# Kernel optimization log

Hardware: AMD Instinct MI355X
Metric: run time of the kernel (lower is better)

Reference implementation:

```python
import jax, jax.numpy as jnp
import numpy as np

CFG = {"dt": 1.0, "T_r": 2.0, "kappa_j": 1.0, "tau_j": 10.0, "gamma_m": 1.0, "R_m": 1.0,
       "tau_m": 20.0, "thresh": 1.0, "tau_tr": 20.0, "tau_data": 10.0,
       "alpha_gen": 0.5, "alpha_disc": 0.5}


def _lif(v, x, tr, j, refrac, ti, cfg):
    """One LIF update for a hidden layer (bPC_SNNLayer.update_state)."""
    dt = cfg["dt"]
    j = j + dt / cfg["tau_j"] * (-cfg["kappa_j"] * j + ti)
    is_refr = refrac > 0
    v_next = v + dt / cfg["tau_m"] * (-cfg["gamma_m"] * v + cfg["R_m"] * j)
    v = jnp.where(is_refr, v, v_next)
    spikes = (v > cfg["thresh"]).astype(v.dtype) * (1.0 - is_refr.astype(v.dtype))
    v = v * (1.0 - spikes)
    refrac = jnp.maximum(refrac - dt, 0.0)
    refrac = jnp.where(spikes > 0, jnp.asarray(cfg["T_r"], v.dtype), refrac)
    tr = tr - tr / cfg["tau_tr"] + spikes  # spike trace (layer.x)
    return v, spikes, tr, j, refrac


def _forward(x_data, y_target, W0, W1, W2, V0, V1, V2, num_steps):
    cfg = CFG
    B = x_data.shape[0]
    d0, d1, d2, d3 = x_data.shape[1], W0.shape[1], W1.shape[1], W2.shape[1]
    dt_ = x_data.dtype
    z = lambda d: jnp.zeros((B, d), dt_)
    state = dict(v1=z(d1), tr1=z(d1), j1=z(d1), r1=z(d1), s1=z(d1),
                 v2=z(d2), tr2=z(d2), j2=z(d2), r2=z(d2), s2=z(d2),
                 eg0=z(d0), eg1=z(d1), eg2=z(d2),
                 ed1=z(d1), ed2=z(d2), ed3=z(d3),
                 z_data=z(d0), z_label=z(d3))
    ag, ad = cfg["alpha_gen"], cfg["alpha_disc"]

    def step(st, _):
        # phase 1: currents into hidden layers 1 and 2 (layers 0/3 are data/label, no-op)
        ti1 = -st["eg1"] + st["ed2"] @ V1 - st["ed1"] + st["eg0"] @ W0
        ti2 = -st["eg2"] + st["ed3"] @ V2 - st["ed2"] + st["eg1"] @ W1
        v1, s1, tr1, j1, r1 = _lif(st["v1"], st["tr1"], st["tr1"], st["j1"], st["r1"], ti1, cfg) if False else _lif(st["v1"], st["tr1"], st["tr1"], st["j1"], st["r1"], ti1, cfg)
        v1, s1, tr1, j1, r1 = _lif(st["v1"], st["tr1"], st["tr1"], st["j1"], st["r1"], ti1, cfg)
        v2, s2, tr2, j2, r2 = _lif(st["v2"], st["tr2"], st["tr2"], st["j2"], st["r2"], ti2, cfg)
        # phase 2: error recomputation (training mode with label clamped)
        z_data = st["z_data"] - st["z_data"] / cfg["tau_data"] + x_data
        z_label = st["z_label"] - st["z_label"] / cfg["tau_data"] + y_target
        eg0 = ag * (z_data - s1 @ W0.T)          # layer 0 generative error
        ed1 = ad * (tr1 - x_data @ V0.T)          # layer 1 discriminative error
        eg1 = ag * (tr1 - s2 @ W1.T)
        ed2 = ad * (tr2 - s1 @ V1.T)
        eg2 = ag * (tr2 - y_target @ W2.T)        # top hidden: label-clamped generative target
        ed3 = ad * (z_label - s2 @ V2.T)          # label layer discriminative error
        return dict(v1=v1, tr1=tr1, j1=j1, r1=r1, s1=s1,
                    v2=v2, tr2=tr2, j2=j2, r2=r2, s2=s2,
                    eg0=eg0, eg1=eg1, eg2=eg2, ed1=ed1, ed2=ed2, ed3=ed3,
                    z_data=z_data, z_label=z_label), None

    final, _ = jax.lax.scan(step, state, None, length=num_steps)
    return final["ed3"]


def setup_inputs() -> dict:
    key = jax.random.key(0)
    ks = jax.random.split(key, 8)
    B = 128
    sizes = (2048, 4096, 4096, 512)
    sc = 0.02  # weight scale kept small so dynamics stay numerically sane over 16 steps
    return {
        "x_data": jax.random.normal(ks[0], (B, sizes[0]), jnp.float32),
        "y_target": jax.random.normal(ks[1], (B, sizes[3]), jnp.float32),
        "W0": jax.random.normal(ks[2], (sizes[0], sizes[1]), jnp.float32) * sc,
        "W1": jax.random.normal(ks[3], (sizes[1], sizes[2]), jnp.float32) * sc,
        "W2": jax.random.normal(ks[4], (sizes[2], sizes[3]), jnp.float32) * sc,
        "V0": jax.random.normal(ks[5], (sizes[1], sizes[0]), jnp.float32) * sc,
        "V1": jax.random.normal(ks[6], (sizes[2], sizes[1]), jnp.float32) * sc,
        "V2": jax.random.normal(ks[7], (sizes[3], sizes[2]), jnp.float32) * sc,
        "num_steps": 16,
    }


def reference(x_data, y_target, W0, W1, W2, V0, V1, V2, num_steps):
    return _forward(x_data, y_target, W0, W1, W2, V0, V1, V2, num_steps)
```

## Files before the change

kernel.cpp:

```cpp
#include <hip/hip_runtime.h>


#define DEVINL __device__ __forceinline__

using bf16x8 = __attribute__((ext_vector_type(8))) __bf16;
using f32x4  = __attribute__((ext_vector_type(4))) float;
using i32x4  = __attribute__((ext_vector_type(4))) int;
typedef unsigned char uchar;

static constexpr int BB = 128;
static constexpr int D0 = 2048, D1 = 4096, D2 = 4096, D3 = 512;
static constexpr int NSTEPS = 16;

struct Ctx {
  const float *x, *y, *W0, *W1, *W2, *V0, *V1, *V2;
  float *v1, *j1, *r1, *tr1, *v2, *j2, *r2, *tr2;
  float *zd, *zl, *xV0T, *yW2T;
  __bf16 *x_bf, *y_bf, *eg0_bf, *eg1_bf, *ed2_bf, *ed3_bf;
  uchar *s1_f8, *s2_f8, *WA8, *WB8;
  __bf16 *W0t, *W1t, *V1t, *V2t, *V0n, *W2n;
  float *out;
};

DEVINL void gload16(const void* g, void* l) {
  __builtin_amdgcn_global_load_lds(
      (const __attribute__((address_space(1))) void*)g,
      (__attribute__((address_space(3))) void*)l, 16, 0, 0);
}
DEVINL uint32_t lds_off(const void* p) {
  return (uint32_t)(uintptr_t)(__attribute__((address_space(3))) const void*)p;
}
DEVINL bf16x8 dsr128(uint32_t addr) {
  i32x4 r;
  asm volatile("ds_read_b128 %0, %1" : "=v"(r) : "v"(addr));
  return __builtin_bit_cast(bf16x8, r);
}
DEVINL long dsr64(uint32_t addr) {
  long r;
  asm volatile("ds_read_b64 %0, %1" : "=v"(r) : "v"(addr));
  return r;
}

struct Seg { const __bf16* A; unsigned ldA; const __bf16* W; unsigned ldW; int iters; };
struct SPtr { const __bf16 *a0, *a1, *w; };
struct SPtrW { const __bf16 *a, *w; };

DEVINL SPtr mkptr(const Seg& s, int t) {
  int r = t >> 3;
  int u = ((t & 7) ^ (r & 7)) * 8;
  SPtr p;
  p.a0 = s.A + (size_t)r * s.ldA + u;
  p.a1 = s.A + (size_t)(r + 32) * s.ldA + u;
  p.w  = s.W + (size_t)r * s.ldW + u;
  return p;
}
DEVINL SPtrW mkptrw(const Seg& s, int t) {
  int r = t >> 3;
  int u = ((t & 7) ^ (r & 7)) * 8;
  SPtrW p;
  p.a = s.A + (size_t)r * s.ldA + u;
  p.w = s.W + (size_t)r * s.ldW + u;
  return p;
}

DEVINL void run_gemm(const Seg* segs, int nIter, __bf16* lsA, __bf16* lsW,
                     int t, int wm, int wn, int l16, int lg, f32x4* acc) {
  const int seg0it = segs[0].iters;
  SPtr p = mkptr(segs[0], t);
  int nxt = 0;
  auto stage = [&](int s) {
    __bf16* bA = lsA + (s & 3) * 4096;
    __bf16* bW = lsW + (s & 3) * 2048;
    gload16(p.a0, bA + t * 8);
    gload16(p.a1, bA + 2048 + t * 8);
    gload16(p.w,  bW + t * 8);
    p.a0 += 64; p.a1 += 64; p.w += 64;
    if (++nxt == seg0it) p = mkptr(segs[1], t);
  };

  const int x7 = l16 & 7;
  uint32_t aB = lds_off(lsA), wB = lds_off(lsW);
  uint32_t aAd[2][2], wAd[2];
#pragma unroll
  for (int mt = 0; mt < 2; ++mt)
#pragma unroll
    for (int ks = 0; ks < 2; ++ks)
      aAd[mt][ks] = aB + (uint32_t)(wm * 32 + mt * 16 + l16) * 128u
                       + (uint32_t)(((ks * 4 + lg) ^ x7) * 16);
#pragma unroll
  for (int ks = 0; ks < 2; ++ks)
    wAd[ks] = wB + (uint32_t)(wn * 16 + l16) * 128u
                 + (uint32_t)(((ks * 4 + lg) ^ x7) * 16);

  auto compute = [&](int i) {
    uint32_t oa = (uint32_t)(i & 3) * 8192u, ow = (uint32_t)(i & 3) * 4096u;
    bf16x8 a00 = dsr128(aAd[0][0] + oa);
    bf16x8 a01 = dsr128(aAd[0][1] + oa);
    bf16x8 a10 = dsr128(aAd[1][0] + oa);
    bf16x8 a11 = dsr128(aAd[1][1] + oa);
    bf16x8 b0  = dsr128(wAd[0] + ow);
    bf16x8 b1  = dsr128(wAd[1] + ow);
    asm volatile("s_waitcnt lgkmcnt(0)" ::: "memory");
    __builtin_amdgcn_sched_barrier(0);
    __builtin_amdgcn_s_setprio(1);
    acc[0] = __builtin_amdgcn_mfma_f32_16x16x32_bf16(a00, b0, acc[0], 0, 0, 0);
    acc[1] = __builtin_amdgcn_mfma_f32_16x16x32_bf16(a10, b0, acc[1], 0, 0, 0);
    acc[0] = __builtin_amdgcn_mfma_f32_16x16x32_bf16(a01, b1, acc[0], 0, 0, 0);
    acc[1] = __builtin_amdgcn_mfma_f32_16x16x32_bf16(a11, b1, acc[1], 0, 0, 0);
    __builtin_amdgcn_s_setprio(0);
  };

  stage(0); stage(1); stage(2);
  for (int i = 0; i < nIter - 3; ++i) {
    asm volatile("s_waitcnt vmcnt(6)" ::: "memory");
    __builtin_amdgcn_s_barrier();
    stage(i + 3);
    compute(i);
  }
  asm volatile("s_waitcnt vmcnt(6)" ::: "memory");
  __builtin_amdgcn_s_barrier();
  compute(nIter - 3);
  asm volatile("s_waitcnt vmcnt(3)" ::: "memory");
  __builtin_amdgcn_s_barrier();
  compute(nIter - 2);
  asm volatile("s_waitcnt vmcnt(0)" ::: "memory");
  __builtin_amdgcn_s_barrier();
  compute(nIter - 1);
}

DEVINL void run_gemm128w(const Seg* segs, int nIter, __bf16* lsA, __bf16* lsW,
                         int t, int wm, int wn, int l16, int lg, f32x4* acc) {
  const int seg0it = segs[0].iters;
  SPtrW p = mkptrw(segs[0], t);
  int nxt = 0;
  auto stage = [&](int buf) {
    __bf16* bA = lsA + buf * 8192;
    __bf16* bW = lsW + buf * 8192;
    gload16(p.a,      bA + t * 8);
    gload16(p.a + 64, bA + 4096 + t * 8);
    gload16(p.w,      bW + t * 8);
    gload16(p.w + 64, bW + 4096 + t * 8);
    p.a += 128; p.w += 128;
    if (++nxt == seg0it) p = mkptrw(segs[1], t);
  };

  const int x7 = l16 & 7;
  uint32_t aB = lds_off(lsA), wB = lds_off(lsW);
  uint32_t aAd[2][2], wAd[2];
#pragma unroll
  for (int mt = 0; mt < 2; ++mt)
#pragma unroll
    for (int ks = 0; ks < 2; ++ks)
      aAd[mt][ks] = aB + (uint32_t)(wm * 32 + mt * 16 + l16) * 128u
                       + (uint32_t)(((ks * 4 + lg) ^ x7) * 16);
#pragma unroll
  for (int ks = 0; ks < 2; ++ks)
    wAd[ks] = wB + (uint32_t)(wn * 16 + l16) * 128u
                 + (uint32_t)(((ks * 4 + lg) ^ x7) * 16);

  auto compute = [&](int buf) {
    uint32_t oa = (uint32_t)buf * 16384u, ow = (uint32_t)buf * 16384u;
    bf16x8 a00 = dsr128(aAd[0][0] + oa);
    bf16x8 a01 = dsr128(aAd[0][1] + oa);
    bf16x8 a10 = dsr128(aAd[1][0] + oa);
    bf16x8 a11 = dsr128(aAd[1][1] + oa);
    bf16x8 b0  = dsr128(wAd[0] + ow);
    bf16x8 b1  = dsr128(wAd[1] + ow);
    bf16x8 c00 = dsr128(aAd[0][0] + oa + 8192);
    bf16x8 c01 = dsr128(aAd[0][1] + oa + 8192);
    bf16x8 c10 = dsr128(aAd[1][0] + oa + 8192);
    bf16x8 c11 = dsr128(aAd[1][1] + oa + 8192);
    bf16x8 d0  = dsr128(wAd[0] + ow + 8192);
    bf16x8 d1  = dsr128(wAd[1] + ow + 8192);
    asm volatile("s_waitcnt lgkmcnt(0)" ::: "memory");
    __builtin_amdgcn_sched_barrier(0);
    __builtin_amdgcn_s_setprio(1);
    acc[0] = __builtin_amdgcn_mfma_f32_16x16x32_bf16(a00, b0, acc[0], 0, 0, 0);
    acc[1] = __builtin_amdgcn_mfma_f32_16x16x32_bf16(a10, b0, acc[1], 0, 0, 0);
    acc[0] = __builtin_amdgcn_mfma_f32_16x16x32_bf16(a01, b1, acc[0], 0, 0, 0);
    acc[1] = __builtin_amdgcn_mfma_f32_16x16x32_bf16(a11, b1, acc[1], 0, 0, 0);
    acc[0] = __builtin_amdgcn_mfma_f32_16x16x32_bf16(c00, d0, acc[0], 0, 0, 0);
    acc[1] = __builtin_amdgcn_mfma_f32_16x16x32_bf16(c10, d0, acc[1], 0, 0, 0);
    acc[0] = __builtin_amdgcn_mfma_f32_16x16x32_bf16(c01, d1, acc[0], 0, 0, 0);
    acc[1] = __builtin_amdgcn_mfma_f32_16x16x32_bf16(c11, d1, acc[1], 0, 0, 0);
    __builtin_amdgcn_s_setprio(0);
  };

  stage(0); stage(1);
  int cur = 0, nx = 2;
  for (int i = 0; i < nIter - 2; ++i) {
    asm volatile("s_waitcnt vmcnt(4)" ::: "memory");
    __builtin_amdgcn_s_barrier();
    stage(nx);
    compute(cur);
    cur = (cur == 2) ? 0 : cur + 1;
    nx  = (nx == 2) ? 0 : nx + 1;
  }
  asm volatile("s_waitcnt vmcnt(4)" ::: "memory");
  __builtin_amdgcn_s_barrier();
  compute(cur);
  cur = (cur == 2) ? 0 : cur + 1;
  asm volatile("s_waitcnt vmcnt(0)" ::: "memory");
  __builtin_amdgcn_s_barrier();
  compute(cur);
}


__global__ __launch_bounds__(512, 1) void phase1_v17(Ctx c, float edsc) {
  __shared__ __align__(16) __bf16 lsA[3][8192];
  __shared__ __align__(16) __bf16 lsW[3][8192];
  int t = threadIdx.x, w = t >> 6, l = t & 63;
  int l16 = l & 15, lg = l >> 4, wm = w >> 2, wn = w & 3;
  int bx = blockIdx.x;
  int z = bx >> 7, idx = bx & 127;
  int mh = idx >> 6, n0 = (idx & 63) * 64;
  f32x4 acc[2];
  f32x4 z4 = {0.f, 0.f, 0.f, 0.f};
  acc[0] = z4; acc[1] = z4;

  Seg segs[2]; int nIter, N;
  float *v, *j, *rf, *tr; const float* aux; const __bf16* buf; uchar* sf8;
  if (z == 0) {
    segs[0] = { c.ed2_bf + (size_t)mh * 64 * D2, (unsigned)D2, c.V1t + (size_t)n0 * D2, (unsigned)D2, 32 };
    segs[1] = { c.eg0_bf + (size_t)mh * 64 * D0, (unsigned)D0, c.W0t + (size_t)n0 * D0, (unsigned)D0, 16 };
    nIter = 48; N = D1;
    v = c.v1; j = c.j1; rf = c.r1; tr = c.tr1; buf = c.eg1_bf; aux = c.xV0T; sf8 = c.s1_f8;
  } else {
    segs[0] = { c.ed3_bf + (size_t)mh * 64 * D3, (unsigned)D3, c.V2t + (size_t)n0 * D3, (unsigned)D3, 4 };
    segs[1] = { c.eg1_bf + (size_t)mh * 64 * D1, (unsigned)D1, c.W1t + (size_t)n0 * D1, (unsigned)D1, 32 };
    nIter = 36; N = D2;
    v = c.v2; j = c.j2; rf = c.r2; tr = c.tr2; buf = c.ed2_bf; aux = c.yW2T; sf8 = c.s2_f8;
  }

  run_gemm128w(segs, nIter, &lsA[0][0], &lsW[0][0], t, wm, wn, l16, lg, acc);

  int n = n0 + wn * 16 + l16;
#pragma unroll
  for (int mt = 0; mt < 2; ++mt) {
#pragma unroll
    for (int r = 0; r < 4; ++r) {
      int b = mh * 64 + wm * 32 + mt * 16 + lg * 4 + r;
      size_t idx2 = (size_t)b * N + n;
      float to = tr[idx2];
      float ti = acc[mt][r] - (float)buf[idx2] - edsc * (to - aux[idx2]);
      float jo = j[idx2];
      float jn = jo + 0.1f * (ti - jo);
      float ro = rf[idx2];
      float vo = v[idx2];
      bool refr = ro > 0.0f;
      float vn = refr ? vo : (vo + 0.05f * (jn - vo));
      float sp = (!refr && vn > 1.0f) ? 1.0f : 0.0f;
      if (sp != 0.0f) vn = 0.0f;
      float rn = fmaxf(ro - 1.0f, 0.0f);
      if (sp != 0.0f) rn = 2.0f;
      float tn = to - 0.05f * to + sp;
      v[idx2] = vn; j[idx2] = jn; rf[idx2] = rn; tr[idx2] = tn;
      sf8[idx2] = (sp != 0.0f) ? (uchar)0x38 : (uchar)0;
    }
  }
}


__global__ __launch_bounds__(256, 2) void phase2_v15(Ctx c) {
  __shared__ __align__(128) uchar lsA[4][8192];
  __shared__ __align__(128) uchar lsW[4][8192];
  int t = threadIdx.x, w = t >> 6, l = t & 63;
  int l16 = l & 15, lg = l >> 4, wm = w >> 1, wn = w & 1;
  int g = blockIdx.x, mh = blockIdx.y;

  const uchar *A, *W; int n0; bool isA;
  if (g < 96) { isA = true;  A = c.s1_f8 + (size_t)mh * 64 * D1; W = c.WA8 + (size_t)g * 64 * 4096;        n0 = g * 64; }
  else        { isA = false; A = c.s2_f8 + (size_t)mh * 64 * D2; W = c.WB8 + (size_t)(g - 96) * 64 * 4096; n0 = (g - 96) * 64; }

  f32x4 acc[4];
  f32x4 z4 = {0.f, 0.f, 0.f, 0.f};
#pragma unroll
  for (int i = 0; i < 4; i++) acc[i] = z4;

  int row8 = t >> 3, u8 = t & 7;
  int su8 = (u8 ^ ((row8 >> 1) & 7)) * 16;
  const uchar* pA0 = A + (size_t)row8 * 4096 + su8;
  const uchar* pA1 = A + (size_t)(row8 + 32) * 4096 + su8;
  const uchar* pW0 = W + (size_t)row8 * 4096 + su8;
  const uchar* pW1 = W + (size_t)(row8 + 32) * 4096 + su8;
  uchar* dA = &lsA[0][0] + t * 16;
  uchar* dW = &lsW[0][0] + t * 16;
  auto stage = [&](int s) {
    uint32_t o = (uint32_t)(s & 3) * 8192u;
    gload16(pA0, dA + o);
    gload16(pA1, dA + o + 4096);
    gload16(pW0, dW + o);
    gload16(pW1, dW + o + 4096);
    pA0 += 128; pA1 += 128; pW0 += 128; pW1 += 128;
  };

  uint32_t aB = lds_off(lsA), wB = lds_off(lsW);
  uint32_t adA[2], adW[2];
#pragma unroll
  for (int mt = 0; mt < 2; ++mt) {
    int ra = wm * 32 + mt * 16 + l16;
    adA[mt] = aB + (uint32_t)ra * 128u
            + (uint32_t)((((lg >> 1) ^ ((ra >> 1) & 7)) * 16) + (lg & 1) * 8);
  }
#pragma unroll
  for (int nt = 0; nt < 2; ++nt) {
    int rw = wn * 32 + nt * 16 + l16;
    adW[nt] = wB + (uint32_t)rw * 128u
            + (uint32_t)((((lg >> 1) ^ ((rw >> 1) & 7)) * 16) + (lg & 1) * 8);
  }

  auto compute = [&](int i) {
    uint32_t off = (uint32_t)(i & 3) * 8192u;
    uint32_t A0 = adA[0] + off, A1 = adA[1] + off;
    uint32_t B0 = adW[0] + off, B1 = adW[1] + off;
    long a0v0 = dsr64(A0);         long a1v0 = dsr64(A1);
    long b0v0 = dsr64(B0);         long b1v0 = dsr64(B1);
    long a0v1 = dsr64(A0 ^ 32u);   long a1v1 = dsr64(A1 ^ 32u);
    long b0v1 = dsr64(B0 ^ 32u);   long b1v1 = dsr64(B1 ^ 32u);
    long a0v2 = dsr64(A0 ^ 64u);   long a1v2 = dsr64(A1 ^ 64u);
    long b0v2 = dsr64(B0 ^ 64u);   long b1v2 = dsr64(B1 ^ 64u);
    long a0v3 = dsr64(A0 ^ 96u);   long a1v3 = dsr64(A1 ^ 96u);
    long b0v3 = dsr64(B0 ^ 96u);   long b1v3 = dsr64(B1 ^ 96u);
    asm volatile("s_waitcnt lgkmcnt(0)" ::: "memory");
    __builtin_amdgcn_sched_barrier(0);
    __builtin_amdgcn_s_setprio(1);
    acc[0] = __builtin_amdgcn_mfma_f32_16x16x32_fp8_fp8(a0v0, b0v0, acc[0], 0, 0, 0);
    acc[1] = __builtin_amdgcn_mfma_f32_16x16x32_fp8_fp8(a0v0, b1v0, acc[1], 0, 0, 0);
    acc[2] = __builtin_amdgcn_mfma_f32_16x16x32_fp8_fp8(a1v0, b0v0, acc[2], 0, 0, 0);
    acc[3] = __builtin_amdgcn_mfma_f32_16x16x32_fp8_fp8(a1v0, b1v0, acc[3], 0, 0, 0);
    acc[0] = __builtin_amdgcn_mfma_f32_16x16x32_fp8_fp8(a0v1, b0v1, acc[0], 0, 0, 0);
    acc[1] = __builtin_amdgcn_mfma_f32_16x16x32_fp8_fp8(a0v1, b1v1, acc[1], 0, 0, 0);
    acc[2] = __builtin_amdgcn_mfma_f32_16x16x32_fp8_fp8(a1v1, b0v1, acc[2], 0, 0, 0);
    acc[3] = __builtin_amdgcn_mfma_f32_16x16x32_fp8_fp8(a1v1, b1v1, acc[3], 0, 0, 0);
    acc[0] = __builtin_amdgcn_mfma_f32_16x16x32_fp8_fp8(a0v2, b0v2, acc[0], 0, 0, 0);
    acc[1] = __builtin_amdgcn_mfma_f32_16x16x32_fp8_fp8(a0v2, b1v2, acc[1], 0, 0, 0);
    acc[2] = __builtin_amdgcn_mfma_f32_16x16x32_fp8_fp8(a1v2, b0v2, acc[2], 0, 0, 0);
    acc[3] = __builtin_amdgcn_mfma_f32_16x16x32_fp8_fp8(a1v2, b1v2, acc[3], 0, 0, 0);
    acc[0] = __builtin_amdgcn_mfma_f32_16x16x32_fp8_fp8(a0v3, b0v3, acc[0], 0, 0, 0);
    acc[1] = __builtin_amdgcn_mfma_f32_16x16x32_fp8_fp8(a0v3, b1v3, acc[1], 0, 0, 0);
    acc[2] = __builtin_amdgcn_mfma_f32_16x16x32_fp8_fp8(a1v3, b0v3, acc[2], 0, 0, 0);
    acc[3] = __builtin_amdgcn_mfma_f32_16x16x32_fp8_fp8(a1v3, b1v3, acc[3], 0, 0, 0);
    __builtin_amdgcn_s_setprio(0);
  };

  const int nIter = 32;
  stage(0); stage(1); stage(2);
  for (int i = 0; i < nIter - 3; ++i) {
    asm volatile("s_waitcnt vmcnt(8)" ::: "memory");
    __builtin_amdgcn_s_barrier();
    stage(i + 3);
    compute(i);
  }
  asm volatile("s_waitcnt vmcnt(8)" ::: "memory");
  __builtin_amdgcn_s_barrier();
  compute(nIter - 3);
  asm volatile("s_waitcnt vmcnt(4)" ::: "memory");
  __builtin_amdgcn_s_barrier();
  compute(nIter - 2);
  asm volatile("s_waitcnt vmcnt(0)" ::: "memory");
  __builtin_amdgcn_s_barrier();
  compute(nIter - 1);

#pragma unroll
  for (int mt = 0; mt < 2; ++mt)
#pragma unroll
    for (int nt = 0; nt < 2; ++nt) {
      int nn = n0 + wn * 32 + nt * 16 + l16;
#pragma unroll
      for (int r = 0; r < 4; ++r) {
        int b = mh * 64 + wm * 32 + mt * 16 + lg * 4 + r;
        float av = acc[mt * 2 + nt][r];
        if (isA) {
          if (nn < 2048) {
            size_t idx = (size_t)b * D0 + nn;
            float zo = c.zd[idx]; float zn = zo - 0.1f * zo + c.x[idx];
            c.zd[idx] = zn;
            c.eg0_bf[idx] = (__bf16)(0.5f * (zn - av));
          } else {
            size_t idx = (size_t)b * D2 + (nn - 2048);
            c.ed2_bf[idx] = (__bf16)(0.5f * (c.tr2[idx] - av));
          }
        } else {
          if (nn < 4096) {
            size_t idx = (size_t)b * D1 + nn;
            c.eg1_bf[idx] = (__bf16)(0.5f * (c.tr1[idx] - av));
          } else {
            size_t idx = (size_t)b * D3 + (nn - 4096);
            float zo = c.zl[idx]; float zn = zo - 0.1f * zo + c.y[idx];
            c.zl[idx] = zn;
            float e = 0.5f * (zn - av);
            c.out[idx] = e; c.ed3_bf[idx] = (__bf16)e;
          }
        }
      }
    }
}


__global__ __launch_bounds__(256, 2) void precomp_v6(Ctx c) {
  __shared__ __align__(16) __bf16 lsA[4][4096];
  __shared__ __align__(16) __bf16 lsW[4][2048];
  int t = threadIdx.x, w = t >> 6, l = t & 63;
  int l16 = l & 15, lg = l >> 4, wm = w >> 1, wn = w & 1;
  int n0 = blockIdx.x * 32, mh = blockIdx.y;
  f32x4 acc[2];
  f32x4 z4 = {0.f, 0.f, 0.f, 0.f};
  acc[0] = z4; acc[1] = z4;

  Seg segs[2]; int nIter, N; float* outp;
  if (blockIdx.z == 0) {
    segs[0] = { c.x_bf + (size_t)mh * 64 * D0, (unsigned)D0, c.V0n + (size_t)n0 * D0, (unsigned)D0, 32 };
    nIter = 32; N = D1; outp = c.xV0T;
  } else {
    segs[0] = { c.y_bf + (size_t)mh * 64 * D3, (unsigned)D3, c.W2n + (size_t)n0 * D3, (unsigned)D3, 8 };
    nIter = 8; N = D2; outp = c.yW2T;
  }
  segs[1] = segs[0];

  run_gemm(segs, nIter, &lsA[0][0], &lsW[0][0], t, wm, wn, l16, lg, acc);

  int n = n0 + wn * 16 + l16;
#pragma unroll
  for (int mt = 0; mt < 2; ++mt)
#pragma unroll
    for (int r = 0; r < 4; ++r) {
      int b = mh * 64 + wm * 32 + mt * 16 + lg * 4 + r;
      outp[(size_t)b * N + n] = acc[mt][r];
    }
}


__global__ __launch_bounds__(256) void wprep_kernel(Ctx c, int g0) {
  __shared__ float ls[64][65];
  int g = blockIdx.x + g0;
  const float* src; __bf16* tp = nullptr; uchar* n8 = nullptr; __bf16* nb = nullptr; int R, C;
  if (g < 2048)       { src = c.W0; n8 = c.WA8;                         tp = c.W0t; R = D0; C = D1; }
  else if (g < 6144)  { g -= 2048;  src = c.W1; n8 = c.WB8;             tp = c.W1t; R = D1; C = D2; }
  else if (g < 10240) { g -= 6144;  src = c.V1; n8 = c.WA8 + (size_t)2048 * 4096; tp = c.V1t; R = D2; C = D1; }
  else if (g < 10752) { g -= 10240; src = c.V2; n8 = c.WB8 + (size_t)4096 * 4096; tp = c.V2t; R = D3; C = D2; }
  else if (g < 12800) { g -= 10752; src = c.V0; nb = c.V0n; R = D1; C = D0; }
  else                { g -= 12800; src = c.W2; nb = c.W2n; R = D2; C = D3; }
  int tpr = C / 64;
  int r0 = (g / tpr) * 64, c0 = (g % tpr) * 64;
  int t = threadIdx.x, r = t >> 2, q = t & 3;

  const float4* s4 = reinterpret_cast<const float4*>(src + (size_t)(r0 + r) * C + c0 + q * 16);
  if (n8) {
    int pk[4];
#pragma unroll
    for (int i = 0; i < 4; i++) {
      float4 v = s4[i];
      ls[r][q * 16 + i * 4 + 0] = v.x; ls[r][q * 16 + i * 4 + 1] = v.y;
      ls[r][q * 16 + i * 4 + 2] = v.z; ls[r][q * 16 + i * 4 + 3] = v.w;
      int wd = __builtin_amdgcn_cvt_pk_fp8_f32(v.x, v.y, 0, false);
      wd = __builtin_amdgcn_cvt_pk_fp8_f32(v.z, v.w, wd, true);
      pk[i] = wd;
    }
    int4 pv; pv.x = pk[0]; pv.y = pk[1]; pv.z = pk[2]; pv.w = pk[3];
    *reinterpret_cast<int4*>(n8 + (size_t)(r0 + r) * C + c0 + q * 16) = pv;
    __syncthreads();
    union { __bf16 h[16]; int4 qq[2]; } wv;
#pragma unroll
    for (int i = 0; i < 16; i++) wv.h[i] = (__bf16)ls[q * 16 + i][r];
    int4* dt = reinterpret_cast<int4*>(tp + (size_t)(c0 + r) * R + r0 + q * 16);
    dt[0] = wv.qq[0]; dt[1] = wv.qq[1];
  } else {
    union { __bf16 h[16]; int4 qq[2]; } uu;
#pragma unroll
    for (int i = 0; i < 4; i++) {
      float4 v = s4[i];
      uu.h[i * 4 + 0] = (__bf16)v.x; uu.h[i * 4 + 1] = (__bf16)v.y;
      uu.h[i * 4 + 2] = (__bf16)v.z; uu.h[i * 4 + 3] = (__bf16)v.w;
    }
    int4* dn = reinterpret_cast<int4*>(nb + (size_t)(r0 + r) * C + c0 + q * 16);
    dn[0] = uu.qq[0]; dn[1] = uu.qq[1];
  }
}

__global__ __launch_bounds__(256) void castinit_kernel(Ctx c) {
  int i = blockIdx.x * 256 + threadIdx.x;
  const int NX = BB * D0 / 4;
  union { __bf16 h[4]; uint2 u; } p, q;
  if (i < NX) {
    float4 xv = reinterpret_cast<const float4*>(c.x)[i];
    reinterpret_cast<float4*>(c.zd)[i] = xv;
    p.h[0] = (__bf16)xv.x; p.h[1] = (__bf16)xv.y; p.h[2] = (__bf16)xv.z; p.h[3] = (__bf16)xv.w;
    reinterpret_cast<uint2*>(c.x_bf)[i] = p.u;
    q.h[0] = (__bf16)(0.5f * xv.x); q.h[1] = (__bf16)(0.5f * xv.y);
    q.h[2] = (__bf16)(0.5f * xv.z); q.h[3] = (__bf16)(0.5f * xv.w);
    reinterpret_cast<uint2*>(c.eg0_bf)[i] = q.u;
  } else {
    int k = i - NX;
    float4 yv = reinterpret_cast<const float4*>(c.y)[k];
    reinterpret_cast<float4*>(c.zl)[k] = yv;
    p.h[0] = (__bf16)yv.x; p.h[1] = (__bf16)yv.y; p.h[2] = (__bf16)yv.z; p.h[3] = (__bf16)yv.w;
    reinterpret_cast<uint2*>(c.y_bf)[k] = p.u;
    q.h[0] = (__bf16)(0.5f * yv.x); q.h[1] = (__bf16)(0.5f * yv.y);
    q.h[2] = (__bf16)(0.5f * yv.z); q.h[3] = (__bf16)(0.5f * yv.w);
    reinterpret_cast<uint2*>(c.ed3_bf)[k] = q.u;
  }
}


extern "C" void kernel_launch(void* const* d_in, const int* in_sizes, int n_in,
                              void* d_out, int out_size, void* d_ws, size_t ws_size,
                              hipStream_t stream) {
  Ctx c;
  c.x  = (const float*)d_in[0];
  c.y  = (const float*)d_in[1];
  c.W0 = (const float*)d_in[2];
  c.W1 = (const float*)d_in[3];
  c.W2 = (const float*)d_in[4];
  c.V0 = (const float*)d_in[5];
  c.V1 = (const float*)d_in[6];
  c.V2 = (const float*)d_in[7];
  c.out = (float*)d_out;

  char* p = (char*)d_ws;
  auto af = [&](size_t n) -> float* { float* r = (float*)p; p += ((n * 4 + 255) & ~(size_t)255); return r; };
  auto ah = [&](size_t n) -> __bf16* { __bf16* r = (__bf16*)p; p += ((n * 2 + 255) & ~(size_t)255); return r; };
  auto au = [&](size_t n) -> uchar* { uchar* r = (uchar*)p; p += ((n + 255) & ~(size_t)255); return r; };

  const size_t S1 = (size_t)BB * D1;
  c.v1 = af(S1); c.j1 = af(S1); c.r1 = af(S1); c.tr1 = af(S1);
  c.v2 = af(S1); c.j2 = af(S1); c.r2 = af(S1); c.tr2 = af(S1);
  c.eg1_bf = ah(S1); c.ed2_bf = ah(S1);
  size_t zero_bytes = (size_t)(p - (char*)d_ws);
  c.zd = af((size_t)BB * D0); c.zl = af((size_t)BB * D3);
  c.xV0T = af(S1); c.yW2T = af(S1);
  c.x_bf = ah((size_t)BB * D0); c.y_bf = ah((size_t)BB * D3);
  c.eg0_bf = ah((size_t)BB * D0); c.ed3_bf = ah((size_t)BB * D3);
  c.s1_f8 = au(S1); c.s2_f8 = au(S1);
  c.W0t = ah((size_t)D0 * D1); c.W1t = ah((size_t)D1 * D2); c.V1t = ah((size_t)D2 * D1); c.V2t = ah((size_t)D3 * D2);
  c.V0n = ah((size_t)D1 * D0); c.W2n = ah((size_t)D2 * D3);
  c.WA8 = au((size_t)(D0 + D2) * 4096);
  c.WB8 = au((size_t)(D1 + D3) * 4096);

  hipMemsetAsync(d_ws, 0, zero_bytes, stream);
  castinit_kernel<<<320, 256, 0, stream>>>(c);
  wprep_kernel<<<3072, 256, 0, stream>>>(c, 10240);
  wprep_kernel<<<4096, 256, 0, stream>>>(c, 2048);
  wprep_kernel<<<4096, 256, 0, stream>>>(c, 6144);
  wprep_kernel<<<2048, 256, 0, stream>>>(c, 0);
  precomp_v6<<<dim3(128, 2, 2), 256, 0, stream>>>(c);

  for (int s = 1; s < NSTEPS; s++) {
    phase1_v17<<<256, 512, 0, stream>>>(c, 0.5f);
    phase2_v15<<<dim3(168, 2), 256, 0, stream>>>(c);
  }
}
```

Baseline: 824.8 us.

## Widen phase2 FP8 GEMM tile to 64x128 with 512-thread blocks

The phase2 FP8 MFMA kernel now uses 512-thread blocks. Each block computes a 64x128 output tile instead of 64x64, with 8 waves arranged 2x4, so each A stripe loaded into LDS is reused across twice as many output columns. The block count halves to 168, with the batch half folded into blockIdx.x. LDS for W doubles and occupancy is bound to one block per CU. Global traffic for the spike matrix drops, in exchange for fewer blocks and possibly lower latency hiding.

After: 867.8 us. 1.05x slower.

```diff
diff --git a/kernel.cpp b/kernel.cpp
--- a/kernel.cpp
+++ b/kernel.cpp
@@ -261,16 +261,17 @@
 }
 
 
-__global__ __launch_bounds__(256, 2) void phase2_v15(Ctx c) {
+__global__ __launch_bounds__(512, 1) void phase2_v19(Ctx c) {
   __shared__ __align__(128) uchar lsA[4][8192];
-  __shared__ __align__(128) uchar lsW[4][8192];
+  __shared__ __align__(128) uchar lsW[4][16384];
   int t = threadIdx.x, w = t >> 6, l = t & 63;
-  int l16 = l & 15, lg = l >> 4, wm = w >> 1, wn = w & 1;
-  int g = blockIdx.x, mh = blockIdx.y;
+  int l16 = l & 15, lg = l >> 4, wm = w >> 2, wn = w & 3;
+  int bx = blockIdx.x;
+  int tile = bx >> 1, mh = bx & 1;
 
   const uchar *A, *W; int n0; bool isA;
-  if (g < 96) { isA = true;  A = c.s1_f8 + (size_t)mh * 64 * D1; W = c.WA8 + (size_t)g * 64 * 4096;        n0 = g * 64; }
-  else        { isA = false; A = c.s2_f8 + (size_t)mh * 64 * D2; W = c.WB8 + (size_t)(g - 96) * 64 * 4096; n0 = (g - 96) * 64; }
+  if (tile < 48) { isA = true;  A = c.s1_f8 + (size_t)mh * 64 * D1; W = c.WA8 + (size_t)tile * 128 * 4096;        n0 = tile * 128; }
+  else           { isA = false; A = c.s2_f8 + (size_t)mh * 64 * D2; W = c.WB8 + (size_t)(tile - 48) * 128 * 4096; n0 = (tile - 48) * 128; }
 
   f32x4 acc[4];
   f32x4 z4 = {0.f, 0.f, 0.f, 0.f};
@@ -279,19 +280,18 @@
 
   int row8 = t >> 3, u8 = t & 7;
   int su8 = (u8 ^ ((row8 >> 1) & 7)) * 16;
-  const uchar* pA0 = A + (size_t)row8 * 4096 + su8;
-  const uchar* pA1 = A + (size_t)(row8 + 32) * 4096 + su8;
+  const uchar* pA  = A + (size_t)row8 * 4096 + su8;
   const uchar* pW0 = W + (size_t)row8 * 4096 + su8;
-  const uchar* pW1 = W + (size_t)(row8 + 32) * 4096 + su8;
+  const uchar* pW1 = W + (size_t)(row8 + 64) * 4096 + su8;
   uchar* dA = &lsA[0][0] + t * 16;
   uchar* dW = &lsW[0][0] + t * 16;
   auto stage = [&](int s) {
-    uint32_t o = (uint32_t)(s & 3) * 8192u;
-    gload16(pA0, dA + o);
-    gload16(pA1, dA + o + 4096);
-    gload16(pW0, dW + o);
-    gload16(pW1, dW + o + 4096);
-    pA0 += 128; pA1 += 128; pW0 += 128; pW1 += 128;
+    uint32_t oA = (uint32_t)(s & 3) * 8192u;
+    uint32_t oW = (uint32_t)(s & 3) * 16384u;
+    gload16(pA,  dA + oA);
+    gload16(pW0, dW + oW);
+    gload16(pW1, dW + oW + 8192u);
+    pA += 128; pW0 += 128; pW1 += 128;
   };
 
   uint32_t aB = lds_off(lsA), wB = lds_off(lsW);
@@ -310,9 +310,10 @@
   }
 
   auto compute = [&](int i) {
-    uint32_t off = (uint32_t)(i & 3) * 8192u;
-    uint32_t A0 = adA[0] + off, A1 = adA[1] + off;
-    uint32_t B0 = adW[0] + off, B1 = adW[1] + off;
+    uint32_t offA = (uint32_t)(i & 3) * 8192u;
+    uint32_t offW = (uint32_t)(i & 3) * 16384u;
+    uint32_t A0 = adA[0] + offA, A1 = adA[1] + offA;
+    uint32_t B0 = adW[0] + offW, B1 = adW[1] + offW;
     long a0v0 = dsr64(A0);         long a1v0 = dsr64(A1);
     long b0v0 = dsr64(B0);         long b1v0 = dsr64(B1);
     long a0v1 = dsr64(A0 ^ 32u);   long a1v1 = dsr64(A1 ^ 32u);
@@ -346,15 +347,15 @@
   const int nIter = 32;
   stage(0); stage(1); stage(2);
   for (int i = 0; i < nIter - 3; ++i) {
-    asm volatile("s_waitcnt vmcnt(8)" ::: "memory");
+    asm volatile("s_waitcnt vmcnt(6)" ::: "memory");
     __builtin_amdgcn_s_barrier();
     stage(i + 3);
     compute(i);
   }
-  asm volatile("s_waitcnt vmcnt(8)" ::: "memory");
+  asm volatile("s_waitcnt vmcnt(6)" ::: "memory");
   __builtin_amdgcn_s_barrier();
   compute(nIter - 3);
-  asm volatile("s_waitcnt vmcnt(4)" ::: "memory");
+  asm volatile("s_waitcnt vmcnt(3)" ::: "memory");
   __builtin_amdgcn_s_barrier();
   compute(nIter - 2);
   asm volatile("s_waitcnt vmcnt(0)" ::: "memory");
@@ -546,6 +547,6 @@
 
   for (int s = 1; s < NSTEPS; s++) {
     phase1_v17<<<256, 512, 0, stream>>>(c, 0.5f);
-    phase2_v15<<<dim3(168, 2), 256, 0, stream>>>(c);
-  }
-}
+    phase2_v19<<<168, 512, 0, stream>>>(c);
+  }
+}
```
